# Kernel optimization log

Measured on AMD Instinct MI355X. Metric: run time of the kernel, lower is better.

Reference implementation:

```python
import jax, jax.numpy as jnp
import numpy as np

H_HEADS = 4

def setup_inputs() -> dict:
    key = jax.random.key(0)
    ks = jax.random.split(key, 14)
    B, C, H, W = 8, 512, 32, 32
    r = C // H_HEADS  # SE reduction = h per SelfModule(channel, h)
    s_in = 0.02
    inp = {
        'x': jax.random.normal(ks[0], (B, C, H, W), jnp.float32),
        'wq': jax.random.normal(ks[1], (C, C), jnp.float32) * s_in,
        'bq': jnp.zeros((C,), jnp.float32),
        'wk': jax.random.normal(ks[2], (C, C), jnp.float32) * s_in,
        'bk': jnp.zeros((C,), jnp.float32),
        'wv': jax.random.normal(ks[3], (C, C), jnp.float32) * s_in,
        'bv': jnp.zeros((C,), jnp.float32),
        'fc1_w': jax.random.normal(ks[4], (r, C), jnp.float32) * s_in,
        'fc1_b': jnp.zeros((r,), jnp.float32),
        'fc2_w': jax.random.normal(ks[5], (C, r), jnp.float32) * s_in,
        'fc2_b': jnp.zeros((C,), jnp.float32),
        'gate_w': jax.random.normal(ks[6], (1, C), jnp.float32) * s_in,
        'gate_b': jnp.zeros((1,), jnp.float32),
    }
    return inp

def _conv1x1(y, w, b):
    # y: [B,C,H,W], w: [O,C] (1x1 conv kernel squeezed), b: [O]
    return jnp.einsum('bchw,oc->bohw', y, w) + b[None, :, None, None]

def reference(x, wq, bq, wk, bk, wv, bv, fc1_w, fc1_b, fc2_w, fc2_b, gate_w, gate_b):
    B, C, H, W = x.shape
    h = H_HEADS
    dk = C // h
    N = H * W

    # --- SelfScaling (SE without final sigmoid-in-block; sigmoid applied at mul) ---
    p = x.mean(axis=(2, 3))                                   # [B,C] global avg pool
    f = jax.nn.relu(p @ fc1_w.T + fc1_b) @ fc2_w.T + fc2_b    # [B,C]
    x = x * jax.nn.sigmoid(f)[:, :, None, None] + x

    # --- RTrans: conv1x1 QKV, attention over flattened H*W ---
    q = _conv1x1(x, wq, bq).reshape(B, h, dk, N).transpose(0, 1, 3, 2)  # [B,h,N,dk]
    k = _conv1x1(x, wk, bk).reshape(B, h, dk, N)                        # [B,h,dk,N]
    v = _conv1x1(x, wv, bv).reshape(B, h, dk, N)                        # [B,h,dk,N]
    scale = 1.0 / float(np.sqrt(dk))
    att = jax.nn.softmax(jnp.einsum('bhnd,bhdm->bhnm', q, k) * scale, axis=-1)  # [B,h,N,N]
    o = jnp.einsum('bhdn,bhnm->bhdm', v, att).reshape(B, C, H, W)  # v @ att as in torch

    # --- SelfGating ---
    gate = jax.nn.sigmoid(_conv1x1(o, gate_w, gate_b))  # [B,1,H,W]
    return o * gate + o
```

## Files before the change

### kernel.cpp

```cpp
#include <hip/hip_runtime.h>
#include <hip/hip_bf16.h>

#define B_ 8
#define C_ 512
#define N_ 1024
#define HEADS_ 4
#define DK_ 128
#define R_ 128

typedef float f32x4 __attribute__((ext_vector_type(4)));
typedef __bf16 bf16x8 __attribute__((ext_vector_type(8)));
typedef short short4v __attribute__((ext_vector_type(4)));
typedef unsigned short u16;

constexpr float kScale = 0.08838834764831845f;

#define OFF_P   0u
#define OFF_SS  16384u
#define OFF_WB  32768u
#define OFF_XT  1605632u
#define OFF_QT  9994240u
#define OFF_KT  18382848u
#define OFF_V   26771456u
#define OFF_DEN 35160064u
#define OFF_G   35291136u

__device__ __forceinline__ u16 f2b(float f) {
  __hip_bfloat16 h = __float2bfloat16(f);
  return __builtin_bit_cast(u16, h);
}

typedef const __attribute__((address_space(1))) unsigned int* gptr_t;
typedef __attribute__((address_space(3))) unsigned int* lptr_t;
__device__ __forceinline__ void gload16(const void* g, void* l) {
  __builtin_amdgcn_global_load_lds((gptr_t)g, (lptr_t)l, 16, 0, 0);
}

__device__ __forceinline__ f32x4 mfma16(bf16x8 a, bf16x8 b, f32x4 c) {
  return __builtin_amdgcn_mfma_f32_16x16x32_bf16(a, b, c, 0, 0, 0);
}

#if __has_builtin(__builtin_amdgcn_mfma_f32_16x16x16bf16_1k)
__device__ __forceinline__ f32x4 mfma_k16(short4v a, short4v b, f32x4 c) {
  return __builtin_amdgcn_mfma_f32_16x16x16bf16_1k(a, b, c, 0, 0, 0);
}
#else
__device__ __forceinline__ f32x4 mfma_k16(short4v a, short4v b, f32x4 c) {
  bf16x8 a8 = {}, b8 = {};
  for (int e = 0; e < 4; e++) {
    ((u16*)&a8)[e] = ((u16*)&a)[e];
    ((u16*)&b8)[e] = ((u16*)&b)[e];
  }
  return __builtin_amdgcn_mfma_f32_16x16x32_bf16(a8, b8, c, 0, 0, 0);
}
#endif

__global__ __launch_bounds__(64) void k_pool(const float* __restrict__ x,
                                             float* __restrict__ p) {
  int bc = blockIdx.x, lane = threadIdx.x;
  const float4* row = (const float4*)(x + (size_t)bc * N_);
  float s = 0.f;
  for (int i = lane; i < N_ / 4; i += 64) {
    float4 t = row[i];
    s += t.x + t.y + t.z + t.w;
  }
  for (int o = 32; o > 0; o >>= 1) s += __shfl_down(s, o, 64);
  if (lane == 0) p[bc] = s * (1.0f / N_);
}

__global__ __launch_bounds__(256) void k_se(const float* __restrict__ p,
                                            const float* __restrict__ fc1w,
                                            const float* __restrict__ fc1b,
                                            const float* __restrict__ fc2w,
                                            const float* __restrict__ fc2b,
                                            float* __restrict__ ss) {
  __shared__ float pl[C_];
  __shared__ float f1[R_];
  int b = blockIdx.x, t = threadIdx.x;
  for (int c = t; c < C_; c += 256) pl[c] = p[b * C_ + c];
  __syncthreads();
  if (t < R_) {
    float a = fc1b[t];
    for (int c = 0; c < C_; c++) a += pl[c] * fc1w[t * C_ + c];
    f1[t] = fmaxf(a, 0.f);
  }
  __syncthreads();
  for (int c = t; c < C_; c += 256) {
    float a = fc2b[c];
    for (int j = 0; j < R_; j++) a += f1[j] * fc2w[c * R_ + j];
    ss[b * C_ + c] = 1.f + 1.f / (1.f + __expf(-a));
  }
}

__global__ __launch_bounds__(256) void k_castw_zero(const float* __restrict__ wq,
                                                    const float* __restrict__ wk,
                                                    const float* __restrict__ wv,
                                                    u16* __restrict__ wb,
                                                    float* __restrict__ g) {
  int bid = blockIdx.x;
  if (bid >= 768) {
    g[(bid - 768) * 256 + threadIdx.x] = 0.f;
    return;
  }
  int i = bid * 256 + threadIdx.x;
  int idx = i * 4;
  const float* srcs[3] = {wq, wk, wv};
  int w = idx / (C_ * C_), off = idx % (C_ * C_);
  float4 v = *(const float4*)(srcs[w] + off);
  u16* d = wb + idx;
  d[0] = f2b(v.x); d[1] = f2b(v.y); d[2] = f2b(v.z); d[3] = f2b(v.w);
}

__global__ __launch_bounds__(256) void k_xt(const float* __restrict__ x,
                                            const float* __restrict__ ss,
                                            u16* __restrict__ xt) {
  int b = blockIdx.z, c0 = blockIdx.y * 64, n0 = blockIdx.x * 64;
  __shared__ float tile[64][65];
  int t = threadIdx.x;
  int cr = t >> 4, nc4 = (t & 15) * 4;
  for (int j = 0; j < 4; j++) {
    int c = cr + j * 16;
    float sc = ss[b * C_ + c0 + c];
    float4 v = *(const float4*)(x + ((size_t)b * C_ + c0 + c) * N_ + n0 + nc4);
    tile[c][nc4 + 0] = v.x * sc;
    tile[c][nc4 + 1] = v.y * sc;
    tile[c][nc4 + 2] = v.z * sc;
    tile[c][nc4 + 3] = v.w * sc;
  }
  __syncthreads();
  int nr = t >> 2, cc = (t & 3) * 16;
  u16 ov[16];
  for (int m = 0; m < 16; m++) ov[m] = f2b(tile[cc + m][nr]);
  u16* dst = xt + ((size_t)b * N_ + n0 + nr) * C_ + c0 + cc;
  for (int m = 0; m < 16; m++) dst[m] = ov[m];
}

__global__ __launch_bounds__(256) void k_qkv(const u16* __restrict__ xt,
                                             const u16* __restrict__ wb,
                                             const float* __restrict__ bq,
                                             const float* __restrict__ bk,
                                             const float* __restrict__ bv,
                                             u16* __restrict__ qt,
                                             u16* __restrict__ kt,
                                             u16* __restrict__ v) {
  __shared__ char smem[32768];
  int b = blockIdx.y / 3, sel = blockIdx.y % 3;
  int tile = blockIdx.x;
  const char *Ab, *Bb;
  u16* out;
  const float* bias;
  int mt, nt, rstride;
  size_t xtoff = (size_t)b * N_ * C_;
  if (sel < 2) {
    mt = tile & 7; nt = tile >> 3;
    Ab = (const char*)(xt + xtoff + (size_t)mt * 128 * C_);
    Bb = (const char*)(wb + (size_t)sel * C_ * C_ + (size_t)nt * 128 * C_);
    out = (sel ? kt : qt) + xtoff;
    bias = sel ? bk : bq;
    rstride = C_ * 2;
  } else {
    mt = tile & 3; nt = tile >> 2;
    Ab = (const char*)(wb + (size_t)2 * C_ * C_ + (size_t)mt * 128 * C_);
    Bb = (const char*)(xt + xtoff + (size_t)nt * 128 * C_);
    out = v + (size_t)b * C_ * N_;
    bias = bv;
    rstride = N_ * 2;
  }
  int t = threadIdx.x, lane = t & 63, wid = t >> 6;
  int wr = wid >> 1, wc = wid & 1;
  const f32x4 z4 = {0.f, 0.f, 0.f, 0.f};
  f32x4 acc[4][4];
  for (int i = 0; i < 4; i++)
    for (int j = 0; j < 4; j++) acc[i][j] = z4;

  char* lA = smem;
  char* lB = smem + 16384;
  for (int ko = 0; ko < C_; ko += 64) {
    __syncthreads();
    for (int i = wid; i < 16; i += 4) {
      int beta = i * 1024 + lane * 16;
      int row = beta >> 7, cb = (beta & 127) ^ ((row & 7) << 4);
      gload16(Ab + (size_t)row * 1024 + ko * 2 + cb, lA + beta);
    }
    for (int i = wid; i < 16; i += 4) {
      int beta = i * 1024 + lane * 16;
      int row = beta >> 7, cb = (beta & 127) ^ ((row & 7) << 4);
      gload16(Bb + (size_t)row * 1024 + ko * 2 + cb, lB + beta);
    }
    __syncthreads();
    for (int ks = 0; ks < 2; ks++) {
      int kb = ks * 64 + (lane >> 4) * 16;
      bf16x8 af[4], bfr[4];
      for (int fi = 0; fi < 4; fi++) {
        int row = wr * 64 + fi * 16 + (lane & 15);
        af[fi] = *(const bf16x8*)(lA + row * 128 + (kb ^ ((row & 7) << 4)));
      }
      for (int fj = 0; fj < 4; fj++) {
        int row = wc * 64 + fj * 16 + (lane & 15);
        bfr[fj] = *(const bf16x8*)(lB + row * 128 + (kb ^ ((row & 7) << 4)));
      }
      for (int fi = 0; fi < 4; fi++)
        for (int fj = 0; fj < 4; fj++)
          acc[fi][fj] = mfma16(af[fi], bfr[fj], acc[fi][fj]);
    }
  }
  __syncthreads();
  for (int fi = 0; fi < 4; fi++)
    for (int fj = 0; fj < 4; fj++) {
      int colb = wc * 64 + fj * 16 + (lane & 15);
      for (int r = 0; r < 4; r++) {
        int rowb = wr * 64 + fi * 16 + (lane >> 4) * 4 + r;
        float bva = (sel < 2) ? bias[nt * 128 + colb] : bias[mt * 128 + rowb];
        float val = acc[fi][fj][r] + bva;
        int byte = rowb * 256 + ((colb * 2) ^ ((rowb & 7) << 4));
        *(u16*)(smem + byte) = f2b(val);
      }
    }
  __syncthreads();
  for (int i = t; i < 2048; i += 256) {
    int row = i >> 4, cb = (i & 15) * 16;
    bf16x8 val = *(const bf16x8*)(smem + row * 256 + (cb ^ ((row & 7) << 4)));
    *(bf16x8*)((char*)out + (size_t)(mt * 128 + row) * rstride + nt * 256 + cb) = val;
  }
}

__global__ __launch_bounds__(256) void k_passA(const u16* __restrict__ qt,
                                               const u16* __restrict__ kt,
                                               float* __restrict__ invden) {
  __shared__ char lK[2][32768];
  int bh = blockIdx.x, nb = blockIdx.y * 64;
  int b = bh >> 2, h = bh & 3;
  const char* qb = (const char*)(qt + (size_t)b * N_ * C_ + h * DK_);
  const char* kb = (const char*)(kt + (size_t)b * N_ * C_ + h * DK_);
  int t = threadIdx.x, lane = t & 63, wid = t >> 6;
  bf16x8 aq[4];
  {
    const char* qr = qb + (size_t)(nb + wid * 16 + (lane & 15)) * (C_ * 2);
    for (int ks = 0; ks < 4; ks++)
      aq[ks] = *(const bf16x8*)(qr + ks * 64 + (lane >> 4) * 16);
  }
  float sacc[4] = {0.f, 0.f, 0.f, 0.f};
  const f32x4 z4 = {0.f, 0.f, 0.f, 0.f};
  for (int i = wid; i < 32; i += 4) {
    int beta = i * 1024 + lane * 16;
    int row = beta >> 8, cb = (beta & 255) ^ ((row & 7) << 4);
    gload16(kb + (size_t)row * (C_ * 2) + cb, lK[0] + beta);
  }
  for (int mc = 0; mc < 8; mc++) {
    int cur = mc & 1;
    __syncthreads();
    if (mc < 7) {
      int mnext = (mc + 1) * 128;
      for (int i = wid; i < 32; i += 4) {
        int beta = i * 1024 + lane * 16;
        int row = beta >> 8, cb = (beta & 255) ^ ((row & 7) << 4);
        gload16(kb + (size_t)(mnext + row) * (C_ * 2) + cb, lK[cur ^ 1] + beta);
      }
    }
    for (int fj = 0; fj < 8; fj++) {
      f32x4 s = z4;
      for (int ks = 0; ks < 4; ks++) {
        int row = fj * 16 + (lane & 15);
        bf16x8 bk_ = *(const bf16x8*)(lK[cur] + row * 256 +
                                      ((ks * 64 + (lane >> 4) * 16) ^ ((row & 7) << 4)));
        s = mfma16(aq[ks], bk_, s);
      }
      for (int r = 0; r < 4; r++) sacc[r] += __expf(s[r] * kScale);
    }
  }
  for (int r = 0; r < 4; r++) {
    float vv = sacc[r];
    for (int m = 1; m < 16; m <<= 1) vv += __shfl_xor(vv, m, 64);
    sacc[r] = vv;
  }
  if ((lane & 15) == 0) {
    int n = nb + wid * 16 + (lane >> 4) * 4;
    for (int r = 0; r < 4; r++) invden[(size_t)bh * N_ + n + r] = 1.f / sacc[r];
  }
}

__global__ __launch_bounds__(256) void k_passB(const u16* __restrict__ qt,
                                               const u16* __restrict__ kt,
                                               const u16* __restrict__ v,
                                               const float* __restrict__ invden,
                                               const float* __restrict__ gw,
                                               float* __restrict__ out,
                                               float* __restrict__ g) {
  __shared__ char lQ[2][16384];
  __shared__ char lV[2][16384];
  __shared__ float gacc[64];
  int bh = blockIdx.x, mb = blockIdx.y * 64;
  int b = bh >> 2, h = bh & 3;
  const char* qb = (const char*)(qt + (size_t)b * N_ * C_ + h * DK_);
  const char* kb = (const char*)(kt + (size_t)b * N_ * C_ + h * DK_);
  const char* vb = (const char*)(v + ((size_t)b * C_ + h * DK_) * N_);
  float* ob = out + ((size_t)b * C_ + h * DK_) * N_ + mb;
  const float* idenb = invden + (size_t)bh * N_;
  int t = threadIdx.x, lane = t & 63, wid = t >> 6;
  bf16x8 bkm[4];
  {
    const char* kr = kb + (size_t)(mb + wid * 16 + (lane & 15)) * (C_ * 2);
    for (int ks = 0; ks < 4; ks++)
      bkm[ks] = *(const bf16x8*)(kr + ks * 64 + (lane >> 4) * 16);
  }
  if (t < 64) gacc[t] = 0.f;
  const f32x4 z4 = {0.f, 0.f, 0.f, 0.f};
  f32x4 oacc[8];
  for (int j = 0; j < 8; j++) oacc[j] = z4;

  for (int i = wid; i < 16; i += 4) {
    int beta = i * 1024 + lane * 16;
    int row = beta >> 8, cb = (beta & 255) ^ ((row & 7) << 4);
    gload16(qb + (size_t)row * (C_ * 2) + cb, lQ[0] + beta);
  }
  for (int i = wid; i < 16; i += 4) {
    int beta = i * 1024 + lane * 16;
    int row = beta >> 7, cb = (beta & 127) ^ ((row & 7) << 4);
    gload16(vb + (size_t)row * (N_ * 2) + cb, lV[0] + beta);
  }

  for (int nc = 0; nc < 16; nc++) {
    int n0 = nc * 64, cur = nc & 1;
    __syncthreads();
    if (nc < 15) {
      int nn = n0 + 64;
      for (int i = wid; i < 16; i += 4) {
        int beta = i * 1024 + lane * 16;
        int row = beta >> 8, cb = (beta & 255) ^ ((row & 7) << 4);
        gload16(qb + (size_t)(nn + row) * (C_ * 2) + cb, lQ[cur ^ 1] + beta);
      }
      for (int i = wid; i < 16; i += 4) {
        int beta = i * 1024 + lane * 16;
        int row = beta >> 7, cb = (beta & 127) ^ ((row & 7) << 4);
        gload16(vb + (size_t)row * (N_ * 2) + nn * 2 + cb, lV[cur ^ 1] + beta);
      }
    }
    for (int fj = 0; fj < 4; fj++) {
      f32x4 s = z4;
      int qrow = fj * 16 + (lane & 15);
      const char* qr = lQ[cur] + qrow * 256;
      int qsw = (qrow & 7) << 4;
      for (int ks = 0; ks < 4; ks++) {
        bf16x8 aq = *(const bf16x8*)(qr + ((ks * 64 + (lane >> 4) * 16) ^ qsw));
        s = mfma16(aq, bkm[ks], s);
      }
      float4 id4 = *(const float4*)(idenb + n0 + fj * 16 + (lane >> 4) * 4);
      short4v pp;
      pp[0] = (short)f2b(__expf(s[0] * kScale) * id4.x);
      pp[1] = (short)f2b(__expf(s[1] * kScale) * id4.y);
      pp[2] = (short)f2b(__expf(s[2] * kScale) * id4.z);
      pp[3] = (short)f2b(__expf(s[3] * kScale) * id4.w);
      __builtin_amdgcn_s_setprio(1);
      for (int fd = 0; fd < 8; fd++) {
        int row = fd * 16 + (lane & 15);
        const char* vr = lV[cur] + row * 128;
        int sw = (row & 7) << 4;
        short4v av = *(const short4v*)(vr + ((fj * 32 + (lane >> 4) * 8) ^ sw));
        oacc[fd] = mfma_k16(av, pp, oacc[fd]);
      }
      __builtin_amdgcn_s_setprio(0);
    }
  }
  __syncthreads();
  float part = 0.f;
  int mcol = wid * 16 + (lane & 15);
  for (int fd = 0; fd < 8; fd++) {
    float4 gwv = *(const float4*)(gw + h * DK_ + fd * 16 + (lane >> 4) * 4);
    float gwa[4] = {gwv.x, gwv.y, gwv.z, gwv.w};
    for (int r = 0; r < 4; r++) {
      float val = oacc[fd][r];
      int d = fd * 16 + (lane >> 4) * 4 + r;
      ob[(size_t)d * N_ + mcol] = val;
      part += gwa[r] * val;
    }
  }
  atomicAdd(&gacc[mcol], part);
  __syncthreads();
  if (t < 64) atomicAdd(&g[(size_t)b * N_ + mb + t], gacc[t]);
}

__global__ __launch_bounds__(256) void k_gate_apply(const float* __restrict__ g,
                                                    const float* __restrict__ gb,
                                                    float* __restrict__ out) {
  size_t i = ((size_t)blockIdx.x * 256 + threadIdx.x) * 4;
  int b = (int)(i / ((size_t)C_ * N_));
  int n = (int)(i & (N_ - 1));
  float4 gv = *(const float4*)(g + (size_t)b * N_ + n);
  float bias = gb[0];
  float4 v = *(float4*)(out + i);
  v.x *= 1.f + 1.f / (1.f + __expf(-(gv.x + bias)));
  v.y *= 1.f + 1.f / (1.f + __expf(-(gv.y + bias)));
  v.z *= 1.f + 1.f / (1.f + __expf(-(gv.z + bias)));
  v.w *= 1.f + 1.f / (1.f + __expf(-(gv.w + bias)));
  *(float4*)(out + i) = v;
}

extern "C" void kernel_launch(void* const* d_in, const int* in_sizes, int n_in,
                              void* d_out, int out_size, void* d_ws, size_t ws_size,
                              hipStream_t stream) {
  const float* x    = (const float*)d_in[0];
  const float* wq   = (const float*)d_in[1];
  const float* bq   = (const float*)d_in[2];
  const float* wk   = (const float*)d_in[3];
  const float* bk   = (const float*)d_in[4];
  const float* wv   = (const float*)d_in[5];
  const float* bv   = (const float*)d_in[6];
  const float* fc1w = (const float*)d_in[7];
  const float* fc1b = (const float*)d_in[8];
  const float* fc2w = (const float*)d_in[9];
  const float* fc2b = (const float*)d_in[10];
  const float* gw   = (const float*)d_in[11];
  const float* gb   = (const float*)d_in[12];
  float* out = (float*)d_out;
  char* ws = (char*)d_ws;

  float* p   = (float*)(ws + OFF_P);
  float* ssc = (float*)(ws + OFF_SS);
  u16* wb  = (u16*)(ws + OFF_WB);
  u16* xt  = (u16*)(ws + OFF_XT);
  u16* qt  = (u16*)(ws + OFF_QT);
  u16* kt  = (u16*)(ws + OFF_KT);
  u16* v   = (u16*)(ws + OFF_V);
  float* den = (float*)(ws + OFF_DEN);
  float* g   = (float*)(ws + OFF_G);

  k_pool<<<B_ * C_, 64, 0, stream>>>(x, p);
  k_castw_zero<<<800, 256, 0, stream>>>(wq, wk, wv, wb, g);
  k_se<<<B_, 256, 0, stream>>>(p, fc1w, fc1b, fc2w, fc2b, ssc);
  k_xt<<<dim3(16, 8, B_), 256, 0, stream>>>(x, ssc, xt);
  k_qkv<<<dim3(32, B_ * 3), 256, 0, stream>>>(xt, wb, bq, bk, bv, qt, kt, v);
  k_passA<<<dim3(32, 16), 256, 0, stream>>>(qt, kt, den);
  k_passB<<<dim3(32, 16), 256, 0, stream>>>(qt, kt, v, den, gw, out, g);
  k_gate_apply<<<B_ * C_ * N_ / 1024, 256, 0, stream>>>(g, gb, out);
}
```

Measured before the change: 134.0 us.

## Load Q fragments directly from global into registers and batch PV MFMAs

Pass B no longer stages Q tiles in double-buffered LDS. Each lane now reads its Q fragments straight from global memory into registers at the start of every chunk, which halves LDS use and removes the LDS reads for Q. The loops are also reordered so all four probability fragments are computed first, followed by a fused 8x4 MFMA loop over V with the setprio hints removed. The trade-off is higher register pressure and global loads that sit exposed on the critical path, since they are not prefetched a chunk ahead.

```diff
diff --git a/kernel.cpp b/kernel.cpp
--- a/kernel.cpp
+++ b/kernel.cpp
@@ -286,7 +286,6 @@
                                                const float* __restrict__ gw,
                                                float* __restrict__ out,
                                                float* __restrict__ g) {
-  __shared__ char lQ[2][16384];
   __shared__ char lV[2][16384];
   __shared__ float gacc[64];
   int bh = blockIdx.x, mb = blockIdx.y * 64;
@@ -310,55 +309,55 @@
 
   for (int i = wid; i < 16; i += 4) {
     int beta = i * 1024 + lane * 16;
-    int row = beta >> 8, cb = (beta & 255) ^ ((row & 7) << 4);
-    gload16(qb + (size_t)row * (C_ * 2) + cb, lQ[0] + beta);
-  }
-  for (int i = wid; i < 16; i += 4) {
-    int beta = i * 1024 + lane * 16;
     int row = beta >> 7, cb = (beta & 127) ^ ((row & 7) << 4);
     gload16(vb + (size_t)row * (N_ * 2) + cb, lV[0] + beta);
   }
+  const char* qlane = qb + (size_t)(lane & 15) * (C_ * 2) + (lane >> 4) * 16;
 
   for (int nc = 0; nc < 16; nc++) {
     int n0 = nc * 64, cur = nc & 1;
     __syncthreads();
+    bf16x8 aq[4][4];
+#pragma unroll
+    for (int fj = 0; fj < 4; fj++) {
+      const char* qr = qlane + (size_t)(n0 + fj * 16) * (C_ * 2);
+#pragma unroll
+      for (int ks = 0; ks < 4; ks++)
+        aq[fj][ks] = *(const bf16x8*)(qr + ks * 64);
+    }
     if (nc < 15) {
       int nn = n0 + 64;
       for (int i = wid; i < 16; i += 4) {
         int beta = i * 1024 + lane * 16;
-        int row = beta >> 8, cb = (beta & 255) ^ ((row & 7) << 4);
-        gload16(qb + (size_t)(nn + row) * (C_ * 2) + cb, lQ[cur ^ 1] + beta);
-      }
-      for (int i = wid; i < 16; i += 4) {
-        int beta = i * 1024 + lane * 16;
         int row = beta >> 7, cb = (beta & 127) ^ ((row & 7) << 4);
         gload16(vb + (size_t)row * (N_ * 2) + nn * 2 + cb, lV[cur ^ 1] + beta);
       }
     }
+    short4v pf[4];
+#pragma unroll
     for (int fj = 0; fj < 4; fj++) {
       f32x4 s = z4;
-      int qrow = fj * 16 + (lane & 15);
-      const char* qr = lQ[cur] + qrow * 256;
-      int qsw = (qrow & 7) << 4;
-      for (int ks = 0; ks < 4; ks++) {
-        bf16x8 aq = *(const bf16x8*)(qr + ((ks * 64 + (lane >> 4) * 16) ^ qsw));
-        s = mfma16(aq, bkm[ks], s);
-      }
+#pragma unroll
+      for (int ks = 0; ks < 4; ks++)
+        s = mfma16(aq[fj][ks], bkm[ks], s);
       float4 id4 = *(const float4*)(idenb + n0 + fj * 16 + (lane >> 4) * 4);
       short4v pp;
       pp[0] = (short)f2b(__expf(s[0] * kScale) * id4.x);
       pp[1] = (short)f2b(__expf(s[1] * kScale) * id4.y);
       pp[2] = (short)f2b(__expf(s[2] * kScale) * id4.z);
       pp[3] = (short)f2b(__expf(s[3] * kScale) * id4.w);
-      __builtin_amdgcn_s_setprio(1);
-      for (int fd = 0; fd < 8; fd++) {
-        int row = fd * 16 + (lane & 15);
-        const char* vr = lV[cur] + row * 128;
-        int sw = (row & 7) << 4;
+      pf[fj] = pp;
+    }
+#pragma unroll
+    for (int fd = 0; fd < 8; fd++) {
+      int row = fd * 16 + (lane & 15);
+      const char* vr = lV[cur] + row * 128;
+      int sw = (row & 7) << 4;
+#pragma unroll
+      for (int fj = 0; fj < 4; fj++) {
         short4v av = *(const short4v*)(vr + ((fj * 32 + (lane >> 4) * 8) ^ sw));
-        oacc[fd] = mfma_k16(av, pp, oacc[fd]);
-      }
-      __builtin_amdgcn_s_setprio(0);
+        oacc[fd] = mfma_k16(av, pf[fj], oacc[fd]);
+      }
     }
   }
   __syncthreads();
```

Result: slower. 165.2 us (+23.3%).
